# Kernel tuning notes

Hardware: AMD Instinct MI355X
Metric: run time of the kernel (lower is better)

## Reference

```python
import jax, jax.numpy as jnp
import numpy as np

DIM = 128
NUM_HEADS = 4
WINDOW = (7, 7)


def _rel_pos_index(wh, ww):
    h = jnp.arange(wh)
    w = jnp.arange(ww)
    idx = jnp.stack(jnp.meshgrid(w, h, indexing='ij'))  # (2, wh, ww)
    flat = idx.reshape(2, -1)                           # (2, n)
    rel = flat[:, :, None] - flat[:, None, :]           # (2, n, n)
    rel = jnp.transpose(rel, (1, 2, 0))                 # (n, n, 2)
    rel = rel.at[:, :, 0].add(wh - 1)
    rel = rel.at[:, :, 1].add(ww - 1)
    rel = rel.at[:, :, 0].multiply(2 * ww - 1)
    return jnp.sum(rel, -1)                             # (n, n)


def setup_inputs() -> dict:
    key = jax.random.key(0)
    ks = jax.random.split(key, 7)
    batch, n, c = 4096, WINDOW[0] * WINDOW[1], DIM
    nw = 64  # windows per image; batch % nw == 0
    return {
        'inputs': jax.random.normal(ks[0], (batch, n, c), jnp.float32),
        'mask': jax.random.normal(ks[1], (nw, n, n), jnp.float32),
        'qkv_w': jax.random.normal(ks[2], (c, 3 * c), jnp.float32) * 0.02,
        'qkv_b': jax.random.normal(ks[3], (3 * c,), jnp.float32) * 0.02,
        'proj_w': jax.random.normal(ks[4], (c, c), jnp.float32) * 0.02,
        'proj_b': jax.random.normal(ks[5], (c,), jnp.float32) * 0.02,
        'rpbt': jax.random.normal(ks[6], ((2 * WINDOW[0] - 1) * (2 * WINDOW[1] - 1), NUM_HEADS), jnp.float32) * 0.02,
    }


def reference(inputs, mask, qkv_w, qkv_b, proj_w, proj_b, rpbt):
    batch, n, c = inputs.shape
    head_dim = DIM // NUM_HEADS
    qkv = inputs @ qkv_w + qkv_b                       # (B, n, 3C)
    qkv = qkv.reshape(batch, n, 3, NUM_HEADS, head_dim)
    qkv = jnp.transpose(qkv, (2, 0, 3, 1, 4))          # (3, B, H, n, d)
    q, k, v = qkv[0], qkv[1], qkv[2]
    q = q * head_dim ** -0.5
    att = jnp.einsum('bhqd,bhkd->bhqk', q, k)          # (B, H, n, n)
    rel_idx = _rel_pos_index(*WINDOW).reshape(-1)
    bias = rpbt[rel_idx].reshape(n, n, NUM_HEADS)      # gather
    att = att + jnp.transpose(bias, (2, 0, 1))[None]   # (B, H, n, n)
    nw = mask.shape[0]
    att = att.reshape(batch // nw, nw, NUM_HEADS, n, n)
    att = att + mask[None, :, None]
    att = att.reshape(batch, NUM_HEADS, n, n)
    att = jax.nn.softmax(att, axis=-1)
    x = jnp.einsum('bhqk,bhkd->bhqd', att, v)          # (B, H, n, d)
    x = jnp.transpose(x, (0, 2, 1, 3)).reshape(batch, n, c)
    return x @ proj_w + proj_b
```

## Files before the change

### kernel.cpp

```cpp
#include <hip/hip_runtime.h>

typedef __bf16 bf16x8 __attribute__((ext_vector_type(8)));
typedef float f32x4 __attribute__((ext_vector_type(4)));
typedef unsigned short us4 __attribute__((ext_vector_type(4)));
typedef short s4 __attribute__((ext_vector_type(4)));

#define SCALE 0.17677669529663687f

__device__ __forceinline__ unsigned short f2bf(float f) {
    union { float f; unsigned u; } v; v.f = f;
    unsigned r = v.u + 0x7FFFu + ((v.u >> 16) & 1u);
    return (unsigned short)(r >> 16);
}

__global__ void wa_prep(const float* __restrict__ qkv_w, const float* __restrict__ proj_w,
                        const float* __restrict__ rpbt, const float* __restrict__ mask,
                        unsigned short* __restrict__ wqkvt, unsigned short* __restrict__ wprojt,
                        float* __restrict__ tab, int use_bm) {
    int idx = blockIdx.x * 256 + threadIdx.x;
    if (idx < 49152) {
        int n = idx >> 7, k = idx & 127;
        wqkvt[idx] = f2bf(qkv_w[k * 384 + n]);
    } else if (idx < 65536) {
        int j = idx - 49152;
        int n = j >> 7, k = j & 127;
        wprojt[j] = f2bf(proj_w[k * 128 + n]);
    } else {
        int j = idx - 65536;
        if (use_bm) {
            if (j < 64 * 4 * 49 * 52) {
                int k = j % 52; int t = j / 52; int q = t % 49; t /= 49;
                int h = t & 3, w = t >> 2;
                float v = 0.f;
                if (k < 49) {
                    int rel = (q / 7 - k / 7 + 6) * 13 + (q % 7 - k % 7 + 6);
                    v = rpbt[rel * 4 + h] + mask[w * 2401 + q * 49 + k];
                }
                tab[j] = v;
            }
        } else {
            if (j < 4 * 49 * 52) {
                int k = j % 52; int t = j / 52; int q = t % 49; int h = t / 49;
                float v = 0.f;
                if (k < 49) {
                    int rel = (q / 7 - k / 7 + 6) * 13 + (q % 7 - k % 7 + 6);
                    v = rpbt[rel * 4 + h];
                }
                tab[j] = v;
            }
        }
    }
}

__global__ __launch_bounds__(512, 4) void wa_main(
    const float* __restrict__ x, const float* __restrict__ mask,
    const float* __restrict__ qkv_b, const float* __restrict__ proj_b,
    const unsigned short* __restrict__ wqkvt, const unsigned short* __restrict__ wprojt,
    const float* __restrict__ tab, int use_bm, float* __restrict__ out)
{
    __shared__ unsigned short xb[64][136];
    __shared__ unsigned short Qs[4][64][40];
    __shared__ unsigned short Ks[4][64][40];
    __shared__ unsigned short Vt[4][32][72];

    const int tid  = threadIdx.x;
    const int wv   = tid >> 6;
    const int lane = tid & 63;
    const int l15  = lane & 15;
    const int l4   = lane >> 4;
    const int b    = blockIdx.x;

    {
        const float* xp = x + (size_t)b * 6272;
        for (int i = tid; i < 1568; i += 512) {
            int row = i >> 5;
            int c0  = (i & 31) << 2;
            f32x4 v = *reinterpret_cast<const f32x4*>(xp + i * 4);
            us4 sv;
            for (int j = 0; j < 4; ++j) sv[j] = f2bf(v[j]);
            *reinterpret_cast<us4*>(&xb[row][c0]) = sv;
        }
        us4 z = (us4)0;
        for (int i = tid; i < 510; i += 512) {
            int row = 49 + i / 34;
            int c0  = (i % 34) << 2;
            *reinterpret_cast<us4*>(&xb[row][c0]) = z;
        }
    }
    __syncthreads();

    {
        bf16x8 afr[4][4];
        for (int m = 0; m < 4; ++m)
            for (int kk = 0; kk < 4; ++kk)
                afr[m][kk] = *reinterpret_cast<const bf16x8*>(&xb[m * 16 + l15][kk * 32 + l4 * 8]);
        f32x4 acc[4][3];
        for (int m = 0; m < 4; ++m)
            for (int n = 0; n < 3; ++n)
                acc[m][n] = (f32x4){0.f, 0.f, 0.f, 0.f};
        for (int n = 0; n < 3; ++n) {
            int col = wv * 48 + n * 16 + l15;
            const unsigned short* wp = wqkvt + col * 128 + l4 * 8;
            for (int kk = 0; kk < 4; ++kk) {
                bf16x8 bw = *reinterpret_cast<const bf16x8*>(wp + kk * 32);
                for (int m = 0; m < 4; ++m)
                    acc[m][n] = __builtin_amdgcn_mfma_f32_16x16x32_bf16(afr[m][kk], bw, acc[m][n], 0, 0, 0);
            }
        }
        for (int n = 0; n < 3; ++n) {
            int col  = wv * 48 + n * 16 + l15;
            float bv = qkv_b[col];
            int sec = col >> 7, c = col & 127, h = c >> 5, hc = c & 31;
            for (int m = 0; m < 4; ++m) {
                int row0 = m * 16 + l4 * 4;
                if (sec == 0) {
                    for (int r = 0; r < 4; ++r) Qs[h][row0 + r][hc] = f2bf(acc[m][n][r] + bv);
                } else if (sec == 1) {
                    for (int r = 0; r < 4; ++r) Ks[h][row0 + r][hc] = f2bf(acc[m][n][r] + bv);
                } else {
                    us4 pv;
                    for (int r = 0; r < 4; ++r) pv[r] = f2bf(acc[m][n][r] + bv);
                    *reinterpret_cast<us4*>(&Vt[h][hc][row0]) = pv;
                }
            }
        }
    }
    __syncthreads();

    {
        const int h = wv >> 1, half = wv & 1;
        bf16x8 kf[4];
        for (int n = 0; n < 4; ++n)
            kf[n] = *reinterpret_cast<const bf16x8*>(&Ks[h][n * 16 + l15][l4 * 8]);
        bf16x8 qf[2];
        for (int m = 0; m < 2; ++m)
            qf[m] = *reinterpret_cast<const bf16x8*>(&Qs[h][(half * 2 + m) * 16 + l15][l4 * 8]);
        f32x4 s[2][4];
        for (int m = 0; m < 2; ++m)
            for (int n = 0; n < 4; ++n) s[m][n] = (f32x4){0.f, 0.f, 0.f, 0.f};
        for (int m = 0; m < 2; ++m)
            for (int n = 0; n < 4; ++n)
                s[m][n] = __builtin_amdgcn_mfma_f32_16x16x32_bf16(kf[n], qf[m], s[m][n], 0, 0, 0);

        const float* tp = tab + (size_t)(use_bm ? ((b & 63) * 4 + h) : h) * (49 * 52);
        const float* mp = mask + (size_t)(b & 63) * 2401;

        s4 pf[2][4];
        for (int m = 0; m < 2; ++m) {
            int qg = (half * 2 + m) * 16 + l15;
            bool qok = qg < 49;
            int qc = qok ? qg : 48;
            float vals[4][4];
            for (int n = 0; n < 4; ++n) {
                f32x4 t = *reinterpret_cast<const f32x4*>(tp + qc * 52 + n * 16 + l4 * 4);
                for (int r = 0; r < 4; ++r) {
                    int k = n * 16 + l4 * 4 + r;
                    float lv = -1e30f;
                    if (qok && k < 49) {
                        float add = t[r];
                        if (!use_bm) add += mp[qg * 49 + k];
                        lv = s[m][n][r] * SCALE + add;
                    }
                    vals[n][r] = lv;
                }
            }
            float mx = -1e30f;
            for (int n = 0; n < 4; ++n)
                for (int r = 0; r < 4; ++r) mx = fmaxf(mx, vals[n][r]);
            mx = fmaxf(mx, __shfl_xor(mx, 16));
            mx = fmaxf(mx, __shfl_xor(mx, 32));
            float p[4][4], sum = 0.f;
            for (int n = 0; n < 4; ++n)
                for (int r = 0; r < 4; ++r) { p[n][r] = __expf(vals[n][r] - mx); sum += p[n][r]; }
            sum += __shfl_xor(sum, 16);
            sum += __shfl_xor(sum, 32);
            float ri = 1.0f / sum;
            for (int n = 0; n < 4; ++n) {
                us4 pk;
                for (int r = 0; r < 4; ++r) pk[r] = f2bf(p[n][r] * ri);
                union { us4 u; s4 v; } cv; cv.u = pk;
                pf[m][n] = cv.v;
            }
        }
        f32x4 xacc[2][2];
        for (int m = 0; m < 2; ++m)
            for (int dt = 0; dt < 2; ++dt) xacc[m][dt] = (f32x4){0.f, 0.f, 0.f, 0.f};
        for (int n = 0; n < 4; ++n)
            for (int dt = 0; dt < 2; ++dt) {
                s4 vf = *reinterpret_cast<const s4*>(&Vt[h][dt * 16 + l15][n * 16 + l4 * 4]);
                for (int m = 0; m < 2; ++m)
                    xacc[m][dt] = __builtin_amdgcn_mfma_f32_16x16x16bf16_1k(pf[m][n], vf, xacc[m][dt], 0, 0, 0);
            }
        for (int m = 0; m < 2; ++m)
            for (int dt = 0; dt < 2; ++dt)
                for (int r = 0; r < 4; ++r)
                    Qs[h][(half * 2 + m) * 16 + l4 * 4 + r][dt * 16 + l15] = f2bf(xacc[m][dt][r]);
    }
    __syncthreads();

    {
        bf16x8 a2[4][4];
        for (int m = 0; m < 4; ++m)
            for (int kk = 0; kk < 4; ++kk)
                a2[m][kk] = *reinterpret_cast<const bf16x8*>(&Qs[kk][m * 16 + l15][l4 * 8]);
        f32x4 o[4];
        for (int m = 0; m < 4; ++m) o[m] = (f32x4){0.f, 0.f, 0.f, 0.f};
        int col = wv * 16 + l15;
        const unsigned short* wp = wprojt + col * 128 + l4 * 8;
        for (int kk = 0; kk < 4; ++kk) {
            bf16x8 bw = *reinterpret_cast<const bf16x8*>(wp + kk * 32);
            for (int m = 0; m < 4; ++m)
                o[m] = __builtin_amdgcn_mfma_f32_16x16x32_bf16(a2[m][kk], bw, o[m], 0, 0, 0);
        }
        float pb = proj_b[col];
        float* op = out + (size_t)b * 6272 + col;
        for (int m = 0; m < 4; ++m)
            for (int r = 0; r < 4; ++r) {
                int row = m * 16 + l4 * 4 + r;
                if (row < 49) op[row * 128] = o[m][r] + pb;
            }
    }
}

extern "C" void kernel_launch(void* const* d_in, const int* in_sizes, int n_in,
                              void* d_out, int out_size, void* d_ws, size_t ws_size,
                              hipStream_t stream) {
    const float* x      = (const float*)d_in[0];
    const float* mask   = (const float*)d_in[1];
    const float* qkv_w  = (const float*)d_in[2];
    const float* qkv_b  = (const float*)d_in[3];
    const float* proj_w = (const float*)d_in[4];
    const float* proj_b = (const float*)d_in[5];
    const float* rpbt   = (const float*)d_in[6];
    float* out = (float*)d_out;

    unsigned short* wqkvt  = (unsigned short*)d_ws;
    unsigned short* wprojt = (unsigned short*)((char*)d_ws + 98304);
    float*          tab    = (float*)((char*)d_ws + 131072);

    const size_t needed_big = 131072 + (size_t)64 * 4 * 49 * 52 * 4;
    int use_bm = (ws_size >= needed_big) ? 1 : 0;
    int total  = 65536 + (use_bm ? 64 * 4 * 49 * 52 : 4 * 49 * 52);

    wa_prep<<<(total + 255) / 256, 256, 0, stream>>>(qkv_w, proj_w, rpbt, mask, wqkvt, wprojt, tab, use_bm);
    wa_main<<<4096, 512, 0, stream>>>(x, mask, qkv_b, proj_b, wqkvt, wprojt, tab, use_bm, out);
}
```

Baseline: 124.8 us.

## Alias shared memory regions with XOR swizzles and stage output for coalesced stores

```diff
diff --git a/kernel.cpp b/kernel.cpp
--- a/kernel.cpp
+++ b/kernel.cpp
@@ -8,9 +8,11 @@
 #define SCALE 0.17677669529663687f
 
 __device__ __forceinline__ unsigned short f2bf(float f) {
-    union { float f; unsigned u; } v; v.f = f;
-    unsigned r = v.u + 0x7FFFu + ((v.u >> 16) & 1u);
-    return (unsigned short)(r >> 16);
+    __bf16 h = (__bf16)f;
+    return __builtin_bit_cast(unsigned short, h);
+}
+__device__ __forceinline__ us4 pack4(float a, float b, float c, float d) {
+    us4 r; r[0] = f2bf(a); r[1] = f2bf(b); r[2] = f2bf(c); r[3] = f2bf(d); return r;
 }
 
 __global__ void wa_prep(const float* __restrict__ qkv_w, const float* __restrict__ proj_w,
@@ -28,8 +30,8 @@
     } else {
         int j = idx - 65536;
         if (use_bm) {
-            if (j < 64 * 4 * 49 * 52) {
-                int k = j % 52; int t = j / 52; int q = t % 49; t /= 49;
+            if (j < 64 * 4 * 49 * 64) {
+                int k = j & 63; int t = j >> 6; int q = t % 49; t /= 49;
                 int h = t & 3, w = t >> 2;
                 float v = 0.f;
                 if (k < 49) {
@@ -39,8 +41,8 @@
                 tab[j] = v;
             }
         } else {
-            if (j < 4 * 49 * 52) {
-                int k = j % 52; int t = j / 52; int q = t % 49; int h = t / 49;
+            if (j < 4 * 49 * 64) {
+                int k = j & 63; int t = j >> 6; int q = t % 49; int h = t / 49;
                 float v = 0.f;
                 if (k < 49) {
                     int rel = (q / 7 - k / 7 + 6) * 13 + (q % 7 - k % 7 + 6);
@@ -52,16 +54,15 @@
     }
 }
 
-__global__ __launch_bounds__(512, 4) void wa_main(
+__global__ __launch_bounds__(512, 6) void wa_main(
     const float* __restrict__ x, const float* __restrict__ mask,
     const float* __restrict__ qkv_b, const float* __restrict__ proj_b,
     const unsigned short* __restrict__ wqkvt, const unsigned short* __restrict__ wprojt,
     const float* __restrict__ tab, int use_bm, float* __restrict__ out)
 {
-    __shared__ unsigned short xb[64][136];
-    __shared__ unsigned short Qs[4][64][40];
-    __shared__ unsigned short Ks[4][64][40];
-    __shared__ unsigned short Vt[4][32][72];
+    __shared__ __align__(16) char smem[16384 + 33792];
+    char* const reg0 = smem;
+    char* const reg1 = smem + 16384;
 
     const int tid  = threadIdx.x;
     const int wv   = tid >> 6;
@@ -71,56 +72,74 @@
     const int b    = blockIdx.x;
 
     {
+        char* xb = reg1;
         const float* xp = x + (size_t)b * 6272;
         for (int i = tid; i < 1568; i += 512) {
             int row = i >> 5;
-            int c0  = (i & 31) << 2;
+            int cb  = (i & 31) * 8;
             f32x4 v = *reinterpret_cast<const f32x4*>(xp + i * 4);
-            us4 sv;
-            for (int j = 0; j < 4; ++j) sv[j] = f2bf(v[j]);
-            *reinterpret_cast<us4*>(&xb[row][c0]) = sv;
-        }
-        us4 z = (us4)0;
-        for (int i = tid; i < 510; i += 512) {
-            int row = 49 + i / 34;
-            int c0  = (i % 34) << 2;
-            *reinterpret_cast<us4*>(&xb[row][c0]) = z;
-        }
-    }
-    __syncthreads();
-
-    {
-        bf16x8 afr[4][4];
-        for (int m = 0; m < 4; ++m)
-            for (int kk = 0; kk < 4; ++kk)
-                afr[m][kk] = *reinterpret_cast<const bf16x8*>(&xb[m * 16 + l15][kk * 32 + l4 * 8]);
-        f32x4 acc[4][3];
-        for (int m = 0; m < 4; ++m)
-            for (int n = 0; n < 3; ++n)
-                acc[m][n] = (f32x4){0.f, 0.f, 0.f, 0.f};
+            *reinterpret_cast<us4*>(xb + row * 256 + (cb ^ ((row & 7) << 4))) =
+                pack4(v[0], v[1], v[2], v[3]);
+        }
+        us4 z = (us4)(unsigned short)0;
+        for (int i = tid; i < 480; i += 512) {
+            int row = 49 + (i >> 5);
+            int cb  = (i & 31) * 8;
+            *reinterpret_cast<us4*>(xb + row * 256 + (cb ^ ((row & 7) << 4))) = z;
+        }
+    }
+    __syncthreads();
+
+    {
+        const char* xb = reg1;
+        f32x4 acc[3][4];
+        for (int n = 0; n < 3; ++n)
+            for (int m = 0; m < 4; ++m) acc[n][m] = (f32x4){0.f, 0.f, 0.f, 0.f};
+        const int col0 = wv * 48 + l15;
+        for (int kk = 0; kk < 4; ++kk) {
+            bf16x8 a[4];
+            for (int m = 0; m < 4; ++m) {
+                int row = m * 16 + l15;
+                a[m] = *reinterpret_cast<const bf16x8*>(
+                    xb + row * 256 + ((kk * 64 + l4 * 16) ^ ((row & 7) << 4)));
+            }
+            for (int n = 0; n < 3; ++n) {
+                bf16x8 bw = *reinterpret_cast<const bf16x8*>(wqkvt + (col0 + n * 16) * 128 + kk * 32 + l4 * 8);
+                for (int m = 0; m < 4; ++m)
+                    acc[n][m] = __builtin_amdgcn_mfma_f32_16x16x32_bf16(a[m], bw, acc[n][m], 0, 0, 0);
+            }
+        }
+        __syncthreads();
+        char* Ks = reg1;
+        char* Vt = reg1 + 16384;
         for (int n = 0; n < 3; ++n) {
-            int col = wv * 48 + n * 16 + l15;
-            const unsigned short* wp = wqkvt + col * 128 + l4 * 8;
-            for (int kk = 0; kk < 4; ++kk) {
-                bf16x8 bw = *reinterpret_cast<const bf16x8*>(wp + kk * 32);
+            int col = col0 + n * 16;
+            int sec = col >> 7, c = col & 127, h = c >> 5, hc = c & 31;
+            float bv = qkv_b[col];
+            if (sec == 0) {
+                float bq = bv * SCALE;
                 for (int m = 0; m < 4; ++m)
-                    acc[m][n] = __builtin_amdgcn_mfma_f32_16x16x32_bf16(afr[m][kk], bw, acc[m][n], 0, 0, 0);
-            }
-        }
-        for (int n = 0; n < 3; ++n) {
-            int col  = wv * 48 + n * 16 + l15;
-            float bv = qkv_b[col];
-            int sec = col >> 7, c = col & 127, h = c >> 5, hc = c & 31;
-            for (int m = 0; m < 4; ++m) {
-                int row0 = m * 16 + l4 * 4;
-                if (sec == 0) {
-                    for (int r = 0; r < 4; ++r) Qs[h][row0 + r][hc] = f2bf(acc[m][n][r] + bv);
-                } else if (sec == 1) {
-                    for (int r = 0; r < 4; ++r) Ks[h][row0 + r][hc] = f2bf(acc[m][n][r] + bv);
-                } else {
-                    us4 pv;
-                    for (int r = 0; r < 4; ++r) pv[r] = f2bf(acc[m][n][r] + bv);
-                    *reinterpret_cast<us4*>(&Vt[h][hc][row0]) = pv;
+                    for (int r = 0; r < 4; ++r) {
+                        int row = m * 16 + l4 * 4 + r;
+                        *reinterpret_cast<unsigned short*>(
+                            reg0 + h * 4096 + row * 64 + ((hc * 2) ^ ((row & 3) << 4)))
+                            = f2bf(acc[n][m][r] * SCALE + bq);
+                    }
+            } else if (sec == 1) {
+                for (int m = 0; m < 4; ++m)
+                    for (int r = 0; r < 4; ++r) {
+                        int row = m * 16 + l4 * 4 + r;
+                        *reinterpret_cast<unsigned short*>(
+                            Ks + h * 4096 + row * 64 + ((hc * 2) ^ ((row & 3) << 4)))
+                            = f2bf(acc[n][m][r] + bv);
+                    }
+            } else {
+                for (int m = 0; m < 4; ++m) {
+                    int tok0 = m * 16 + l4 * 4;
+                    *reinterpret_cast<us4*>(
+                        Vt + h * 4096 + hc * 128 + ((tok0 * 2) ^ ((hc & 15) << 3)))
+                        = pack4(acc[n][m][0] + bv, acc[n][m][1] + bv,
+                                acc[n][m][2] + bv, acc[n][m][3] + bv);
                 }
             }
         }
@@ -129,12 +148,19 @@
 
     {
         const int h = wv >> 1, half = wv & 1;
-        bf16x8 kf[4];
-        for (int n = 0; n < 4; ++n)
-            kf[n] = *reinterpret_cast<const bf16x8*>(&Ks[h][n * 16 + l15][l4 * 8]);
-        bf16x8 qf[2];
-        for (int m = 0; m < 2; ++m)
-            qf[m] = *reinterpret_cast<const bf16x8*>(&Qs[h][(half * 2 + m) * 16 + l15][l4 * 8]);
+        const char* Ks = reg1;
+        const char* Vt = reg1 + 16384;
+        bf16x8 kf[4], qf[2];
+        for (int n = 0; n < 4; ++n) {
+            int row = n * 16 + l15;
+            kf[n] = *reinterpret_cast<const bf16x8*>(
+                Ks + h * 4096 + row * 64 + ((l4 * 16) ^ ((row & 3) << 4)));
+        }
+        for (int m = 0; m < 2; ++m) {
+            int row = (half * 2 + m) * 16 + l15;
+            qf[m] = *reinterpret_cast<const bf16x8*>(
+                reg0 + h * 4096 + row * 64 + ((l4 * 16) ^ ((row & 3) << 4)));
+        }
         f32x4 s[2][4];
         for (int m = 0; m < 2; ++m)
             for (int n = 0; n < 4; ++n) s[m][n] = (f32x4){0.f, 0.f, 0.f, 0.f};
@@ -142,24 +168,25 @@
             for (int n = 0; n < 4; ++n)
                 s[m][n] = __builtin_amdgcn_mfma_f32_16x16x32_bf16(kf[n], qf[m], s[m][n], 0, 0, 0);
 
-        const float* tp = tab + (size_t)(use_bm ? ((b & 63) * 4 + h) : h) * (49 * 52);
+        const float* tp = tab + (size_t)(use_bm ? ((b & 63) * 4 + h) : h) * (49 * 64);
         const float* mp = mask + (size_t)(b & 63) * 2401;
 
         s4 pf[2][4];
         for (int m = 0; m < 2; ++m) {
-            int qg = (half * 2 + m) * 16 + l15;
-            bool qok = qg < 49;
+            int tile = half * 2 + m;
+            int qg = tile * 16 + l15;
+            bool qok = (tile < 3) || (l15 == 0);
             int qc = qok ? qg : 48;
+            const float* trow = tp + qc * 64 + l4 * 4;
             float vals[4][4];
             for (int n = 0; n < 4; ++n) {
-                f32x4 t = *reinterpret_cast<const f32x4*>(tp + qc * 52 + n * 16 + l4 * 4);
+                f32x4 t = *reinterpret_cast<const f32x4*>(trow + n * 16);
                 for (int r = 0; r < 4; ++r) {
-                    int k = n * 16 + l4 * 4 + r;
+                    bool kok = (n < 3) || ((l4 | r) == 0);
                     float lv = -1e30f;
-                    if (qok && k < 49) {
-                        float add = t[r];
-                        if (!use_bm) add += mp[qg * 49 + k];
-                        lv = s[m][n][r] * SCALE + add;
+                    if (qok && kok) {
+                        lv = s[m][n][r] + t[r];
+                        if (!use_bm) lv += mp[qg * 49 + n * 16 + l4 * 4 + r];
                     }
                     vals[n][r] = lv;
                 }
@@ -174,51 +201,69 @@
                 for (int r = 0; r < 4; ++r) { p[n][r] = __expf(vals[n][r] - mx); sum += p[n][r]; }
             sum += __shfl_xor(sum, 16);
             sum += __shfl_xor(sum, 32);
-            float ri = 1.0f / sum;
-            for (int n = 0; n < 4; ++n) {
-                us4 pk;
-                for (int r = 0; r < 4; ++r) pk[r] = f2bf(p[n][r] * ri);
-                union { us4 u; s4 v; } cv; cv.u = pk;
-                pf[m][n] = cv.v;
-            }
+            float ri = __builtin_amdgcn_rcpf(sum);
+            for (int n = 0; n < 4; ++n)
+                pf[m][n] = __builtin_bit_cast(s4,
+                    pack4(p[n][0] * ri, p[n][1] * ri, p[n][2] * ri, p[n][3] * ri));
         }
         f32x4 xacc[2][2];
         for (int m = 0; m < 2; ++m)
             for (int dt = 0; dt < 2; ++dt) xacc[m][dt] = (f32x4){0.f, 0.f, 0.f, 0.f};
         for (int n = 0; n < 4; ++n)
             for (int dt = 0; dt < 2; ++dt) {
-                s4 vf = *reinterpret_cast<const s4*>(&Vt[h][dt * 16 + l15][n * 16 + l4 * 4]);
+                s4 vf = *reinterpret_cast<const s4*>(
+                    Vt + h * 4096 + (dt * 16 + l15) * 128 + ((n * 32 + l4 * 8) ^ (l15 << 3)));
                 for (int m = 0; m < 2; ++m)
                     xacc[m][dt] = __builtin_amdgcn_mfma_f32_16x16x16bf16_1k(pf[m][n], vf, xacc[m][dt], 0, 0, 0);
             }
+        __syncthreads();
         for (int m = 0; m < 2; ++m)
             for (int dt = 0; dt < 2; ++dt)
-                for (int r = 0; r < 4; ++r)
-                    Qs[h][(half * 2 + m) * 16 + l4 * 4 + r][dt * 16 + l15] = f2bf(xacc[m][dt][r]);
-    }
-    __syncthreads();
-
-    {
-        bf16x8 a2[4][4];
-        for (int m = 0; m < 4; ++m)
-            for (int kk = 0; kk < 4; ++kk)
-                a2[m][kk] = *reinterpret_cast<const bf16x8*>(&Qs[kk][m * 16 + l15][l4 * 8]);
+                for (int r = 0; r < 4; ++r) {
+                    int row = (half * 2 + m) * 16 + l4 * 4 + r;
+                    int col = h * 32 + dt * 16 + l15;
+                    *reinterpret_cast<unsigned short*>(
+                        reg0 + row * 256 + ((col * 2) ^ ((row & 7) << 4))) = f2bf(xacc[m][dt][r]);
+                }
+    }
+    __syncthreads();
+
+    {
+        const int col = wv * 16 + l15;
         f32x4 o[4];
         for (int m = 0; m < 4; ++m) o[m] = (f32x4){0.f, 0.f, 0.f, 0.f};
-        int col = wv * 16 + l15;
-        const unsigned short* wp = wprojt + col * 128 + l4 * 8;
         for (int kk = 0; kk < 4; ++kk) {
-            bf16x8 bw = *reinterpret_cast<const bf16x8*>(wp + kk * 32);
+            bf16x8 a[4];
+            for (int m = 0; m < 4; ++m) {
+                int row = m * 16 + l15;
+                a[m] = *reinterpret_cast<const bf16x8*>(
+                    reg0 + row * 256 + ((kk * 64 + l4 * 16) ^ ((row & 7) << 4)));
+            }
+            bf16x8 bw = *reinterpret_cast<const bf16x8*>(wprojt + col * 128 + kk * 32 + l4 * 8);
             for (int m = 0; m < 4; ++m)
-                o[m] = __builtin_amdgcn_mfma_f32_16x16x32_bf16(a2[m][kk], bw, o[m], 0, 0, 0);
+                o[m] = __builtin_amdgcn_mfma_f32_16x16x32_bf16(a[m], bw, o[m], 0, 0, 0);
         }
         float pb = proj_b[col];
-        float* op = out + (size_t)b * 6272 + col;
+        float* outb = (float*)reg1;
         for (int m = 0; m < 4; ++m)
             for (int r = 0; r < 4; ++r) {
                 int row = m * 16 + l4 * 4 + r;
-                if (row < 49) op[row * 128] = o[m][r] + pb;
-            }
+                outb[row * 132 + col] = o[m][r] + pb;
+            }
+    }
+    __syncthreads();
+    {
+        const float* outb = (const float*)reg1;
+        float* op = out + (size_t)b * 6272;
+        for (int i = tid; i < 1568; i += 512) {
+            int row = i >> 5, c0 = (i & 31) << 2;
+            f32x4 v; 
+            v[0] = outb[row * 132 + c0 + 0];
+            v[1] = outb[row * 132 + c0 + 1];
+            v[2] = outb[row * 132 + c0 + 2];
+            v[3] = outb[row * 132 + c0 + 3];
+            *reinterpret_cast<f32x4*>(op + i * 4) = v;
+        }
     }
 }
 
@@ -238,9 +283,9 @@
     unsigned short* wprojt = (unsigned short*)((char*)d_ws + 98304);
     float*          tab    = (float*)((char*)d_ws + 131072);
 
-    const size_t needed_big = 131072 + (size_t)64 * 4 * 49 * 52 * 4;
+    const size_t needed_big = 131072 + (size_t)64 * 4 * 49 * 64 * 4;
     int use_bm = (ws_size >= needed_big) ? 1 : 0;
-    int total  = 65536 + (use_bm ? 64 * 4 * 49 * 52 : 4 * 49 * 52);
+    int total  = 65536 + (use_bm ? 64 * 4 * 49 * 64 : 4 * 49 * 64);
 
     wa_prep<<<(total + 255) / 256, 256, 0, stream>>>(qkv_w, proj_w, rpbt, mask, wqkvt, wprojt, tab, use_bm);
     wa_main<<<4096, 512, 0, stream>>>(x, mask, qkv_b, proj_b, wqkvt, wprojt, tab, use_bm, out);
```

After: 220.7 us. 76.9% more time.

## Switch windowed attention to 32x32x16 MFMA tiles with swizzled shared memory

Applied to the files above, without the earlier changes.

```diff
diff --git a/kernel.cpp b/kernel.cpp
--- a/kernel.cpp
+++ b/kernel.cpp
@@ -2,15 +2,16 @@
 
 typedef __bf16 bf16x8 __attribute__((ext_vector_type(8)));
 typedef float f32x4 __attribute__((ext_vector_type(4)));
-typedef unsigned short us4 __attribute__((ext_vector_type(4)));
-typedef short s4 __attribute__((ext_vector_type(4)));
+typedef float f32x16 __attribute__((ext_vector_type(16)));
 
 #define SCALE 0.17677669529663687f
 
 __device__ __forceinline__ unsigned short f2bf(float f) {
-    union { float f; unsigned u; } v; v.f = f;
-    unsigned r = v.u + 0x7FFFu + ((v.u >> 16) & 1u);
-    return (unsigned short)(r >> 16);
+    __bf16 h = (__bf16)f;
+    return __builtin_bit_cast(unsigned short, h);
+}
+__device__ __forceinline__ unsigned pk2(float lo, float hi) {
+    return (unsigned)f2bf(lo) | ((unsigned)f2bf(hi) << 16);
 }
 
 __global__ void wa_prep(const float* __restrict__ qkv_w, const float* __restrict__ proj_w,
@@ -28,8 +29,8 @@
     } else {
         int j = idx - 65536;
         if (use_bm) {
-            if (j < 64 * 4 * 49 * 52) {
-                int k = j % 52; int t = j / 52; int q = t % 49; t /= 49;
+            if (j < 64 * 4 * 49 * 64) {
+                int k = j & 63; int t = j >> 6; int q = t % 49; t /= 49;
                 int h = t & 3, w = t >> 2;
                 float v = 0.f;
                 if (k < 49) {
@@ -39,8 +40,8 @@
                 tab[j] = v;
             }
         } else {
-            if (j < 4 * 49 * 52) {
-                int k = j % 52; int t = j / 52; int q = t % 49; int h = t / 49;
+            if (j < 4 * 49 * 64) {
+                int k = j & 63; int t = j >> 6; int q = t % 49; int h = t / 49;
                 float v = 0.f;
                 if (k < 49) {
                     int rel = (q / 7 - k / 7 + 6) * 13 + (q % 7 - k % 7 + 6);
@@ -52,173 +53,212 @@
     }
 }
 
-__global__ __launch_bounds__(512, 4) void wa_main(
+__global__ __launch_bounds__(512, 6) void wa_main(
     const float* __restrict__ x, const float* __restrict__ mask,
     const float* __restrict__ qkv_b, const float* __restrict__ proj_b,
     const unsigned short* __restrict__ wqkvt, const unsigned short* __restrict__ wprojt,
     const float* __restrict__ tab, int use_bm, float* __restrict__ out)
 {
-    __shared__ unsigned short xb[64][136];
-    __shared__ unsigned short Qs[4][64][40];
-    __shared__ unsigned short Ks[4][64][40];
-    __shared__ unsigned short Vt[4][32][72];
+    __shared__ __align__(16) char smem[49152];
+    char* const Qs = smem;
+    char* const Ks = smem + 16384;
+    char* const Vt = smem + 32768;
 
     const int tid  = threadIdx.x;
     const int wv   = tid >> 6;
     const int lane = tid & 63;
-    const int l15  = lane & 15;
-    const int l4   = lane >> 4;
+    const int l31  = lane & 31;
+    const int hi   = lane >> 5;
     const int b    = blockIdx.x;
 
     {
-        const float* xp = x + (size_t)b * 6272;
-        for (int i = tid; i < 1568; i += 512) {
-            int row = i >> 5;
-            int c0  = (i & 31) << 2;
-            f32x4 v = *reinterpret_cast<const f32x4*>(xp + i * 4);
-            us4 sv;
-            for (int j = 0; j < 4; ++j) sv[j] = f2bf(v[j]);
-            *reinterpret_cast<us4*>(&xb[row][c0]) = sv;
-        }
-        us4 z = (us4)0;
-        for (int i = tid; i < 510; i += 512) {
-            int row = 49 + i / 34;
-            int c0  = (i % 34) << 2;
-            *reinterpret_cast<us4*>(&xb[row][c0]) = z;
+        const int rt   = wv >> 2;
+        const int c4   = wv & 3;
+        const int arow = rt * 32 + l31;
+
+        bf16x8 a[8];
+        if (arow < 49) {
+            const float* xp = x + (size_t)b * 6272 + arow * 128 + hi * 8;
+            #pragma unroll
+            for (int kk = 0; kk < 8; ++kk) {
+                f32x4 v0 = *reinterpret_cast<const f32x4*>(xp + kk * 16);
+                f32x4 v1 = *reinterpret_cast<const f32x4*>(xp + kk * 16 + 4);
+                union { unsigned u[4]; bf16x8 v; } cv;
+                cv.u[0] = pk2(v0[0], v0[1]);
+                cv.u[1] = pk2(v0[2], v0[3]);
+                cv.u[2] = pk2(v1[0], v1[1]);
+                cv.u[3] = pk2(v1[2], v1[3]);
+                a[kk] = cv.v;
+            }
+        } else {
+            #pragma unroll
+            for (int kk = 0; kk < 8; ++kk) a[kk] = (bf16x8)(__bf16)0.0f;
+        }
+
+        #pragma unroll
+        for (int t = 0; t < 3; ++t) {
+            const int ct   = c4 + t * 4;
+            const int colg = ct * 32 + l31;
+            f32x16 acc;
+            #pragma unroll
+            for (int i = 0; i < 16; ++i) acc[i] = 0.f;
+            #pragma unroll
+            for (int kk = 0; kk < 8; ++kk) {
+                bf16x8 bw = *reinterpret_cast<const bf16x8*>(wqkvt + colg * 128 + kk * 16 + hi * 8);
+                acc = __builtin_amdgcn_mfma_f32_32x32x16_bf16(a[kk], bw, acc, 0, 0, 0);
+            }
+            float bv = qkv_b[colg];
+            if (t == 0) {
+                float bq = bv * SCALE;
+                #pragma unroll
+                for (int r = 0; r < 16; ++r) {
+                    int row = rt * 32 + (r & 3) + 8 * (r >> 2) + 4 * hi;
+                    *reinterpret_cast<unsigned short*>(
+                        Qs + c4 * 4096 + row * 64 + ((l31 * 2) ^ ((row & 3) << 4)))
+                        = f2bf(acc[r] * SCALE + bq);
+                }
+            } else if (t == 1) {
+                #pragma unroll
+                for (int r = 0; r < 16; ++r) {
+                    int row = rt * 32 + (r & 3) + 8 * (r >> 2) + 4 * hi;
+                    *reinterpret_cast<unsigned short*>(
+                        Ks + c4 * 4096 + row * 64 + ((l31 * 2) ^ ((row & 3) << 4)))
+                        = f2bf(acc[r] + bv);
+                }
+            } else {
+                #pragma unroll
+                for (int r = 0; r < 16; ++r) {
+                    int tok = rt * 32 + (r & 3) + 8 * (r >> 2) + 4 * hi;
+                    *reinterpret_cast<unsigned short*>(
+                        Vt + c4 * 4096 + l31 * 128 + ((tok * 2) ^ ((l31 & 7) << 4)))
+                        = f2bf(acc[r] + bv);
+                }
+            }
         }
     }
     __syncthreads();
 
     {
-        bf16x8 afr[4][4];
-        for (int m = 0; m < 4; ++m)
-            for (int kk = 0; kk < 4; ++kk)
-                afr[m][kk] = *reinterpret_cast<const bf16x8*>(&xb[m * 16 + l15][kk * 32 + l4 * 8]);
-        f32x4 acc[4][3];
-        for (int m = 0; m < 4; ++m)
-            for (int n = 0; n < 3; ++n)
-                acc[m][n] = (f32x4){0.f, 0.f, 0.f, 0.f};
-        for (int n = 0; n < 3; ++n) {
-            int col = wv * 48 + n * 16 + l15;
-            const unsigned short* wp = wqkvt + col * 128 + l4 * 8;
-            for (int kk = 0; kk < 4; ++kk) {
-                bf16x8 bw = *reinterpret_cast<const bf16x8*>(wp + kk * 32);
-                for (int m = 0; m < 4; ++m)
-                    acc[m][n] = __builtin_amdgcn_mfma_f32_16x16x32_bf16(afr[m][kk], bw, acc[m][n], 0, 0, 0);
-            }
-        }
-        for (int n = 0; n < 3; ++n) {
-            int col  = wv * 48 + n * 16 + l15;
-            float bv = qkv_b[col];
-            int sec = col >> 7, c = col & 127, h = c >> 5, hc = c & 31;
-            for (int m = 0; m < 4; ++m) {
-                int row0 = m * 16 + l4 * 4;
-                if (sec == 0) {
-                    for (int r = 0; r < 4; ++r) Qs[h][row0 + r][hc] = f2bf(acc[m][n][r] + bv);
-                } else if (sec == 1) {
-                    for (int r = 0; r < 4; ++r) Ks[h][row0 + r][hc] = f2bf(acc[m][n][r] + bv);
-                } else {
-                    us4 pv;
-                    for (int r = 0; r < 4; ++r) pv[r] = f2bf(acc[m][n][r] + bv);
-                    *reinterpret_cast<us4*>(&Vt[h][hc][row0]) = pv;
-                }
-            }
+        const int h2 = wv >> 1, qh = wv & 1;
+        const int q  = qh * 32 + l31;
+
+        f32x16 S0, S1;
+        #pragma unroll
+        for (int i = 0; i < 16; ++i) { S0[i] = 0.f; S1[i] = 0.f; }
+        #pragma unroll
+        for (int s = 0; s < 2; ++s) {
+            const int off = s * 32 + hi * 16;
+            bf16x8 qf = *reinterpret_cast<const bf16x8*>(
+                Qs + h2 * 4096 + q * 64 + (off ^ ((q & 3) << 4)));
+            bf16x8 k0 = *reinterpret_cast<const bf16x8*>(
+                Ks + h2 * 4096 + l31 * 64 + (off ^ ((l31 & 3) << 4)));
+            bf16x8 k1 = *reinterpret_cast<const bf16x8*>(
+                Ks + h2 * 4096 + (32 + l31) * 64 + (off ^ ((l31 & 3) << 4)));
+            S0 = __builtin_amdgcn_mfma_f32_32x32x16_bf16(k0, qf, S0, 0, 0, 0);
+            S1 = __builtin_amdgcn_mfma_f32_32x32x16_bf16(k1, qf, S1, 0, 0, 0);
+        }
+
+        const float* tp = tab + (size_t)(use_bm ? ((b & 63) * 4 + h2) : h2) * (49 * 64);
+        const float* mp = mask + (size_t)(b & 63) * 2401;
+        const bool qv = q < 49;
+        const int qc = qv ? q : 48;
+        const float* trow = tp + qc * 64;
+
+        float mx = -1e30f;
+        #pragma unroll
+        for (int g = 0; g < 4; ++g) {
+            f32x4 t0 = *reinterpret_cast<const f32x4*>(trow + g * 8 + hi * 4);
+            f32x4 t1 = *reinterpret_cast<const f32x4*>(trow + 32 + g * 8 + hi * 4);
+            #pragma unroll
+            for (int e = 0; e < 4; ++e) {
+                float v0 = S0[g * 4 + e] + t0[e];
+                float v1 = S1[g * 4 + e] + t1[e];
+                if (!use_bm) {
+                    v0 += mp[qc * 49 + g * 8 + hi * 4 + e];
+                    int k1i = 32 + g * 8 + hi * 4 + e;
+                    if (k1i < 49) v1 += mp[qc * 49 + k1i];
+                }
+                v0 = qv ? v0 : -1e30f;
+                v1 = (qv && (g * 8 + hi * 4 + e) < 17) ? v1 : -1e30f;
+                S0[g * 4 + e] = v0;  mx = fmaxf(mx, v0);
+                S1[g * 4 + e] = v1;  mx = fmaxf(mx, v1);
+            }
+        }
+        mx = fmaxf(mx, __shfl_xor(mx, 32));
+        float sum = 0.f;
+        #pragma unroll
+        for (int i = 0; i < 16; ++i) {
+            float e0 = __expf(S0[i] - mx);
+            float e1 = __expf(S1[i] - mx);
+            S0[i] = e0; S1[i] = e1;
+            sum += e0 + e1;
+        }
+        sum += __shfl_xor(sum, 32);
+        float ri = __builtin_amdgcn_rcpf(sum);
+
+        unsigned pp[2][4][2];
+        #pragma unroll
+        for (int g = 0; g < 4; ++g) {
+            pp[0][g][0] = pk2(S0[g * 4 + 0] * ri, S0[g * 4 + 1] * ri);
+            pp[0][g][1] = pk2(S0[g * 4 + 2] * ri, S0[g * 4 + 3] * ri);
+            pp[1][g][0] = pk2(S1[g * 4 + 0] * ri, S1[g * 4 + 1] * ri);
+            pp[1][g][1] = pk2(S1[g * 4 + 2] * ri, S1[g * 4 + 3] * ri);
+        }
+
+        f32x16 X;
+        #pragma unroll
+        for (int i = 0; i < 16; ++i) X[i] = 0.f;
+        const bool lo = (hi == 0);
+        #pragma unroll
+        for (int s = 0; s < 4; ++s) {
+            const int kt = s >> 1, u = (s & 1) * 2;
+            unsigned a0 = pp[kt][u][0],     a1 = pp[kt][u][1];
+            unsigned b0 = pp[kt][u + 1][0], b1 = pp[kt][u + 1][1];
+            unsigned sa0 = (unsigned)__shfl_xor((int)a0, 32);
+            unsigned sa1 = (unsigned)__shfl_xor((int)a1, 32);
+            unsigned sb0 = (unsigned)__shfl_xor((int)b0, 32);
+            unsigned sb1 = (unsigned)__shfl_xor((int)b1, 32);
+            union { unsigned u4[4]; bf16x8 v; } A;
+            A.u4[0] = lo ? a0  : sb0;
+            A.u4[1] = lo ? a1  : sb1;
+            A.u4[2] = lo ? sa0 : b0;
+            A.u4[3] = lo ? sa1 : b1;
+            bf16x8 Bf = *reinterpret_cast<const bf16x8*>(
+                Vt + h2 * 4096 + l31 * 128 + ((s * 32 + hi * 16) ^ ((l31 & 7) << 4)));
+            X = __builtin_amdgcn_mfma_f32_32x32x16_bf16(A.v, Bf, X, 0, 0, 0);
+        }
+        __syncthreads();
+        #pragma unroll
+        for (int r = 0; r < 16; ++r) {
+            int row = qh * 32 + (r & 3) + 8 * (r >> 2) + 4 * hi;
+            int col = h2 * 32 + l31;
+            *reinterpret_cast<unsigned short*>(
+                Qs + row * 256 + ((col * 2) ^ ((row & 7) << 4))) = f2bf(X[r]);
         }
     }
     __syncthreads();
 
     {
-        const int h = wv >> 1, half = wv & 1;
-        bf16x8 kf[4];
-        for (int n = 0; n < 4; ++n)
-            kf[n] = *reinterpret_cast<const bf16x8*>(&Ks[h][n * 16 + l15][l4 * 8]);
-        bf16x8 qf[2];
-        for (int m = 0; m < 2; ++m)
-            qf[m] = *reinterpret_cast<const bf16x8*>(&Qs[h][(half * 2 + m) * 16 + l15][l4 * 8]);
-        f32x4 s[2][4];
-        for (int m = 0; m < 2; ++m)
-            for (int n = 0; n < 4; ++n) s[m][n] = (f32x4){0.f, 0.f, 0.f, 0.f};
-        for (int m = 0; m < 2; ++m)
-            for (int n = 0; n < 4; ++n)
-                s[m][n] = __builtin_amdgcn_mfma_f32_16x16x32_bf16(kf[n], qf[m], s[m][n], 0, 0, 0);
-
-        const float* tp = tab + (size_t)(use_bm ? ((b & 63) * 4 + h) : h) * (49 * 52);
-        const float* mp = mask + (size_t)(b & 63) * 2401;
-
-        s4 pf[2][4];
-        for (int m = 0; m < 2; ++m) {
-            int qg = (half * 2 + m) * 16 + l15;
-            bool qok = qg < 49;
-            int qc = qok ? qg : 48;
-            float vals[4][4];
-            for (int n = 0; n < 4; ++n) {
-                f32x4 t = *reinterpret_cast<const f32x4*>(tp + qc * 52 + n * 16 + l4 * 4);
-                for (int r = 0; r < 4; ++r) {
-                    int k = n * 16 + l4 * 4 + r;
-                    float lv = -1e30f;
-                    if (qok && k < 49) {
-                        float add = t[r];
-                        if (!use_bm) add += mp[qg * 49 + k];
-                        lv = s[m][n][r] * SCALE + add;
-                    }
-                    vals[n][r] = lv;
-                }
-            }
-            float mx = -1e30f;
-            for (int n = 0; n < 4; ++n)
-                for (int r = 0; r < 4; ++r) mx = fmaxf(mx, vals[n][r]);
-            mx = fmaxf(mx, __shfl_xor(mx, 16));
-            mx = fmaxf(mx, __shfl_xor(mx, 32));
-            float p[4][4], sum = 0.f;
-            for (int n = 0; n < 4; ++n)
-                for (int r = 0; r < 4; ++r) { p[n][r] = __expf(vals[n][r] - mx); sum += p[n][r]; }
-            sum += __shfl_xor(sum, 16);
-            sum += __shfl_xor(sum, 32);
-            float ri = 1.0f / sum;
-            for (int n = 0; n < 4; ++n) {
-                us4 pk;
-                for (int r = 0; r < 4; ++r) pk[r] = f2bf(p[n][r] * ri);
-                union { us4 u; s4 v; } cv; cv.u = pk;
-                pf[m][n] = cv.v;
-            }
-        }
-        f32x4 xacc[2][2];
-        for (int m = 0; m < 2; ++m)
-            for (int dt = 0; dt < 2; ++dt) xacc[m][dt] = (f32x4){0.f, 0.f, 0.f, 0.f};
-        for (int n = 0; n < 4; ++n)
-            for (int dt = 0; dt < 2; ++dt) {
-                s4 vf = *reinterpret_cast<const s4*>(&Vt[h][dt * 16 + l15][n * 16 + l4 * 4]);
-                for (int m = 0; m < 2; ++m)
-                    xacc[m][dt] = __builtin_amdgcn_mfma_f32_16x16x16bf16_1k(pf[m][n], vf, xacc[m][dt], 0, 0, 0);
-            }
-        for (int m = 0; m < 2; ++m)
-            for (int dt = 0; dt < 2; ++dt)
-                for (int r = 0; r < 4; ++r)
-                    Qs[h][(half * 2 + m) * 16 + l4 * 4 + r][dt * 16 + l15] = f2bf(xacc[m][dt][r]);
-    }
-    __syncthreads();
-
-    {
-        bf16x8 a2[4][4];
-        for (int m = 0; m < 4; ++m)
-            for (int kk = 0; kk < 4; ++kk)
-                a2[m][kk] = *reinterpret_cast<const bf16x8*>(&Qs[kk][m * 16 + l15][l4 * 8]);
-        f32x4 o[4];
-        for (int m = 0; m < 4; ++m) o[m] = (f32x4){0.f, 0.f, 0.f, 0.f};
-        int col = wv * 16 + l15;
-        const unsigned short* wp = wprojt + col * 128 + l4 * 8;
-        for (int kk = 0; kk < 4; ++kk) {
-            bf16x8 bw = *reinterpret_cast<const bf16x8*>(wp + kk * 32);
-            for (int m = 0; m < 4; ++m)
-                o[m] = __builtin_amdgcn_mfma_f32_16x16x32_bf16(a2[m][kk], bw, o[m], 0, 0, 0);
-        }
-        float pb = proj_b[col];
-        float* op = out + (size_t)b * 6272 + col;
-        for (int m = 0; m < 4; ++m)
-            for (int r = 0; r < 4; ++r) {
-                int row = m * 16 + l4 * 4 + r;
-                if (row < 49) op[row * 128] = o[m][r] + pb;
-            }
+        const int prt = wv >> 2, pct = wv & 3;
+        const int xrow = prt * 32 + l31;
+        f32x16 o;
+        #pragma unroll
+        for (int i = 0; i < 16; ++i) o[i] = 0.f;
+        #pragma unroll
+        for (int kk = 0; kk < 8; ++kk) {
+            bf16x8 af = *reinterpret_cast<const bf16x8*>(
+                Qs + xrow * 256 + ((kk * 32 + hi * 16) ^ ((xrow & 7) << 4)));
+            bf16x8 bw = *reinterpret_cast<const bf16x8*>(
+                wprojt + (pct * 32 + l31) * 128 + kk * 16 + hi * 8);
+            o = __builtin_amdgcn_mfma_f32_32x32x16_bf16(af, bw, o, 0, 0, 0);
+        }
+        float pb = proj_b[pct * 32 + l31];
+        float* op = out + (size_t)b * 6272 + pct * 32 + l31;
+        #pragma unroll
+        for (int r = 0; r < 16; ++r) {
+            int row = prt * 32 + (r & 3) + 8 * (r >> 2) + 4 * hi;
+            if (row < 49) op[row * 128] = o[r] + pb;
+        }
     }
 }
 
@@ -238,9 +278,9 @@
     unsigned short* wprojt = (unsigned short*)((char*)d_ws + 98304);
     float*          tab    = (float*)((char*)d_ws + 131072);
 
-    const size_t needed_big = 131072 + (size_t)64 * 4 * 49 * 52 * 4;
+    const size_t needed_big = 131072 + (size_t)64 * 4 * 49 * 64 * 4;
     int use_bm = (ws_size >= needed_big) ? 1 : 0;
-    int total  = 65536 + (use_bm ? 64 * 4 * 49 * 52 : 4 * 49 * 52);
+    int total  = 65536 + (use_bm ? 64 * 4 * 49 * 64 : 4 * 49 * 64);
 
     wa_prep<<<(total + 255) / 256, 256, 0, stream>>>(qkv_w, proj_w, rpbt, mask, wqkvt, wprojt, tab, use_bm);
     wa_main<<<4096, 512, 0, stream>>>(x, mask, qkv_b, proj_b, wqkvt, wprojt, tab, use_bm, out);
```

Result: slower. 206.9 us (+65.8%).
